# Optimization experiments

Measured on AMD Instinct MI355X. Metric: run time of the kernel, lower is better.

The kernel has to match this reference:

```python
import jax, jax.numpy as jnp
import numpy as np

E = 768
H = 12
D = E // H
K = 512  # max_relative_positions
SCALE = 1.0 / np.sqrt(3.0 * D)


def setup_inputs() -> dict:
    key = jax.random.key(0)
    ks = jax.random.split(key, 14)
    B, S = 4, 1024
    def lin(kw):
        return jax.random.normal(kw, (E, E), dtype=jnp.float32) * 0.02
    inp = {
        "x": jax.random.normal(ks[0], (B, S, E), dtype=jnp.float32),
        "Wq": lin(ks[1]), "bq": jnp.zeros((E,), jnp.float32),
        "Wk": lin(ks[2]), "bk": jnp.zeros((E,), jnp.float32),
        "Wv": lin(ks[3]), "bv": jnp.zeros((E,), jnp.float32),
        "Wpq": lin(ks[4]), "bpq": jnp.zeros((E,), jnp.float32),
        "Wpk": lin(ks[5]), "bpk": jnp.zeros((E,), jnp.float32),
        "rel_emb": jax.random.normal(ks[6], (2 * K + 1, E), dtype=jnp.float32) * 0.02,
        "Wo": lin(ks[7]), "bo": jnp.zeros((E,), jnp.float32),
    }
    return inp


def reference(x, Wq, bq, Wk, bk, Wv, bv, Wpq, bpq, Wpk, bpk, rel_emb, Wo, bo):
    B, S, _ = x.shape

    def split_heads(y):  # [B,S,E] -> [B,H,S,D]
        return y.reshape(B, S, H, D).transpose(0, 2, 1, 3)

    q_c = split_heads(x @ Wq.T + bq)
    k_c = split_heads(x @ Wk.T + bk)
    v = split_heads(x @ Wv.T + bv)

    # positional projections: [2K+1, E] -> [H, 2K+1, D]
    q_r = (rel_emb @ Wpq.T + bpq).reshape(2 * K + 1, H, D).transpose(1, 0, 2)
    k_r = (rel_emb @ Wpk.T + bpk).reshape(2 * K + 1, H, D).transpose(1, 0, 2)

    # relative index: rel[i, j] = clip(j - i, -K, K) + K
    pos = jnp.arange(S)
    rel = jnp.clip(pos[None, :] - pos[:, None], -K, K) + K  # [S, S] int32
    rel_b = jnp.broadcast_to(rel[None, None], (B, H, S, S))

    # content-to-content: [B,H,S,S]
    attn_cc = jnp.einsum('bhid,bhjd->bhij', q_c, k_c)

    # content-to-position: scores over all 2K+1 rel positions, then gather
    cp_score = jnp.einsum('bhid,hjd->bhij', q_c, k_r)  # [B,H,S,2K+1]
    attn_cp = jnp.take_along_axis(cp_score, rel_b, axis=-1)  # [B,H,S,S]

    # position-to-content: gather along last dim then transpose (i<->j)
    pc_score = jnp.einsum('bhjd,hkd->bhjk', k_c, q_r)  # [B,H,S,2K+1]
    attn_pc = jnp.take_along_axis(pc_score, rel_b, axis=-1).swapaxes(-1, -2)

    scores = (attn_cc + attn_cp + attn_pc) * SCALE
    weights = jax.nn.softmax(scores, axis=-1)

    ctx = jnp.einsum('bhij,bhjd->bhid', weights, v)
    ctx = ctx.transpose(0, 2, 1, 3).reshape(B, S, E)
    return ctx @ Wo.T + bo
```

## Files before the change

### kernel.cpp

```cpp
#include <hip/hip_runtime.h>
#include <stdint.h>

typedef __attribute__((ext_vector_type(8))) short bf8_t;
typedef __attribute__((ext_vector_type(4))) float f4_t;

#define DEV __device__ __forceinline__

constexpr int S_ = 1024;
constexpr float SCALE2_ = 0.104117584f;

DEV float bf2f(unsigned short u) { union { unsigned int i; float f; } v; v.i = ((unsigned int)u) << 16; return v.f; }
DEV unsigned short f2bf(float f) {
  union { float fv; unsigned int i; } v; v.fv = f;
  unsigned int r = v.i + 0x7FFFu + ((v.i >> 16) & 1u);
  return (unsigned short)(r >> 16);
}

DEV void gll16(const unsigned short* g, unsigned short* l) {
  __builtin_amdgcn_global_load_lds(
      (const __attribute__((address_space(1))) unsigned int*)g,
      (__attribute__((address_space(3))) unsigned int*)l, 16, 0, 0);
}

DEV const bf8_t* chunk128(const unsigned short* base, int row, int ck) {
  return (const bf8_t*)((const char*)base + row * 128 + (((ck ^ row) & 7) << 4));
}

struct CvtArgs { const float* src[8]; unsigned short* dst[8]; int nchunks[8]; };

__global__ __launch_bounds__(256) void cvt_kernel(CvtArgs a, int total) {
  int idx = blockIdx.x * 256 + threadIdx.x;
  int step = gridDim.x * 256;
  for (; idx < total; idx += step) {
    int c = idx, s = 0;
    while (c >= a.nchunks[s]) { c -= a.nchunks[s]; ++s; }
    float4 v = ((const float4*)a.src[s])[c];
    ushort4 o;
    o.x = f2bf(v.x); o.y = f2bf(v.y); o.z = f2bf(v.z); o.w = f2bf(v.w);
    ((ushort4*)a.dst[s])[c] = o;
  }
}

__global__ __launch_bounds__(256) void gemm_qkvrel(
    const unsigned short* __restrict__ xb, const unsigned short* __restrict__ Wqkv,
    const unsigned short* __restrict__ relb, const unsigned short* __restrict__ Wrel,
    unsigned short* __restrict__ Cqkv, unsigned short* __restrict__ Crel,
    const float* __restrict__ bq, const float* __restrict__ bk, const float* __restrict__ bv,
    const float* __restrict__ bpq, const float* __restrict__ bpk)
{
  __shared__ unsigned short At[64 * 64];
  __shared__ unsigned short Bt[128 * 64];
  const int tid = threadIdx.x, lane = tid & 63, w = tid >> 6;
  const int li = lane & 15, g = lane >> 4;
  const int wr = w >> 1, wc = w & 1;

  const int bid = blockIdx.x;
  const bool qkv = bid < 1152;
  const unsigned short *A, *B;
  int m0, n0, M, N;
  if (qkv) { m0 = (bid / 18) * 64; n0 = (bid % 18) * 128; A = xb;   B = Wqkv; M = 4096; N = 2304; }
  else     { int t = bid - 1152;
             m0 = (t / 12) * 64;  n0 = (t % 12) * 128;  A = relb; B = Wrel; M = 1025; N = 1536; }

  const int srow = tid >> 3;
  const int sl = (tid & 7) ^ (srow & 7);
  const long aoff0 = (long)min(m0 + srow,      M - 1) * 768 + sl * 8;
  const long aoff1 = (long)min(m0 + srow + 32, M - 1) * 768 + sl * 8;
  const long boff0 = (long)min(n0 + srow,      N - 1) * 768 + sl * 8;
  const long boff1 = (long)min(n0 + srow + 32, N - 1) * 768 + sl * 8;
  const long boff2 = (long)min(n0 + srow + 64, N - 1) * 768 + sl * 8;
  const long boff3 = (long)min(n0 + srow + 96, N - 1) * 768 + sl * 8;

  f4_t acc[2][4];
#pragma unroll
  for (int i = 0; i < 2; ++i)
#pragma unroll
    for (int j = 0; j < 4; ++j) acc[i][j] = f4_t{0.f, 0.f, 0.f, 0.f};

  for (int k0 = 0; k0 < 768; k0 += 64) {
    gll16(A + aoff0 + k0, At + tid * 8);
    gll16(A + aoff1 + k0, At + tid * 8 + 2048);
    gll16(B + boff0 + k0, Bt + tid * 8);
    gll16(B + boff1 + k0, Bt + tid * 8 + 2048);
    gll16(B + boff2 + k0, Bt + tid * 8 + 4096);
    gll16(B + boff3 + k0, Bt + tid * 8 + 6144);
    asm volatile("s_waitcnt vmcnt(0)" ::: "memory");
    __syncthreads();
#pragma unroll
    for (int ks = 0; ks < 2; ++ks) {
      bf8_t a[2], b[4];
#pragma unroll
      for (int fm = 0; fm < 2; ++fm)
        a[fm] = *chunk128(At, wr * 32 + fm * 16 + li, ks * 4 + g);
#pragma unroll
      for (int fn = 0; fn < 4; ++fn)
        b[fn] = *chunk128(Bt, wc * 64 + fn * 16 + li, ks * 4 + g);
#pragma unroll
      for (int fm = 0; fm < 2; ++fm)
#pragma unroll
        for (int fn = 0; fn < 4; ++fn)
          acc[fm][fn] = __builtin_amdgcn_mfma_f32_16x16x32_bf16(a[fm], b[fn], acc[fm][fn], 0, 0, 0);
    }
    __syncthreads();
  }

#pragma unroll
  for (int fm = 0; fm < 2; ++fm)
#pragma unroll
    for (int fn = 0; fn < 4; ++fn)
#pragma unroll
      for (int r = 0; r < 4; ++r) {
        int m = m0 + wr * 32 + fm * 16 + g * 4 + r;
        int n = n0 + wc * 64 + fn * 16 + li;
        if (m >= M || n >= N) continue;
        float v = acc[fm][fn][r];
        if (qkv) {
          int sel = (n >= 1536) ? 2 : (n >= 768 ? 1 : 0);
          int nn = n - sel * 768;
          v += (sel == 0 ? bq : sel == 1 ? bk : bv)[nn];
          long off = (long)sel * 3145728 + (long)((m >> 10) * 12 + (nn >> 6)) * 65536;
          if (sel == 2) off += (nn & 63) * 1024 + (m & 1023);
          else          off += (m & 1023) * 64 + (nn & 63);
          Cqkv[off] = f2bf(v);
        } else {
          int sel = n >= 768 ? 1 : 0;
          int nn = n - sel * 768;
          v += (sel ? bpk : bpq)[nn];
          long off = (long)sel * 787200 + (long)(nn >> 6) * 65600 + (long)m * 64 + (nn & 63);
          Crel[off] = f2bf(v);
        }
      }
}

__global__ __launch_bounds__(256) void gemm_out(
    const unsigned short* __restrict__ A,
    const unsigned short* __restrict__ B,
    float* __restrict__ C, const float* __restrict__ b0)
{
  __shared__ unsigned short At[64 * 64];
  __shared__ unsigned short Bt[128 * 64];
  const int tid = threadIdx.x, lane = tid & 63, w = tid >> 6;
  const int li = lane & 15, g = lane >> 4;
  const int wr = w >> 1, wc = w & 1;
  const int m0 = blockIdx.y * 64, n0 = blockIdx.x * 128;

  const int srow = tid >> 3;
  const int sl = (tid & 7) ^ (srow & 7);
  const long aoff0 = (long)(m0 + srow) * 768 + sl * 8;
  const long aoff1 = (long)(m0 + srow + 32) * 768 + sl * 8;
  const long boff0 = (long)(n0 + srow) * 768 + sl * 8;
  const long boff1 = (long)(n0 + srow + 32) * 768 + sl * 8;
  const long boff2 = (long)(n0 + srow + 64) * 768 + sl * 8;
  const long boff3 = (long)(n0 + srow + 96) * 768 + sl * 8;

  f4_t acc[2][4];
#pragma unroll
  for (int i = 0; i < 2; ++i)
#pragma unroll
    for (int j = 0; j < 4; ++j) acc[i][j] = f4_t{0.f, 0.f, 0.f, 0.f};

  for (int k0 = 0; k0 < 768; k0 += 64) {
    gll16(A + aoff0 + k0, At + tid * 8);
    gll16(A + aoff1 + k0, At + tid * 8 + 2048);
    gll16(B + boff0 + k0, Bt + tid * 8);
    gll16(B + boff1 + k0, Bt + tid * 8 + 2048);
    gll16(B + boff2 + k0, Bt + tid * 8 + 4096);
    gll16(B + boff3 + k0, Bt + tid * 8 + 6144);
    asm volatile("s_waitcnt vmcnt(0)" ::: "memory");
    __syncthreads();
#pragma unroll
    for (int ks = 0; ks < 2; ++ks) {
      bf8_t a[2], b[4];
#pragma unroll
      for (int fm = 0; fm < 2; ++fm)
        a[fm] = *chunk128(At, wr * 32 + fm * 16 + li, ks * 4 + g);
#pragma unroll
      for (int fn = 0; fn < 4; ++fn)
        b[fn] = *chunk128(Bt, wc * 64 + fn * 16 + li, ks * 4 + g);
#pragma unroll
      for (int fm = 0; fm < 2; ++fm)
#pragma unroll
        for (int fn = 0; fn < 4; ++fn)
          acc[fm][fn] = __builtin_amdgcn_mfma_f32_16x16x32_bf16(a[fm], b[fn], acc[fm][fn], 0, 0, 0);
    }
    __syncthreads();
  }

#pragma unroll
  for (int fm = 0; fm < 2; ++fm)
#pragma unroll
    for (int fn = 0; fn < 4; ++fn)
#pragma unroll
      for (int r = 0; r < 4; ++r) {
        int m = m0 + wr * 32 + fm * 16 + g * 4 + r;
        int n = n0 + wc * 64 + fn * 16 + li;
        C[(long)m * 768 + n] = acc[fm][fn][r] + b0[n];
      }
}

__global__ __launch_bounds__(256) void flash_kernel(
    const unsigned short* __restrict__ Q, const unsigned short* __restrict__ Kc,
    const unsigned short* __restrict__ kr, const unsigned short* __restrict__ qr,
    const unsigned short* __restrict__ Vt, unsigned short* __restrict__ ctx)
{
  const int flat = blockIdx.x;
  const int logical = (flat & 7) * 96 + (flat >> 3);
  const int bh = logical >> 4, h = bh % 12, bb = bh / 12;
  const int i0 = (logical & 15) * 64;
  const int tid = threadIdx.x, lane = tid & 63, w = tid >> 6;
  const int g = lane >> 4, li = lane & 15;
  const unsigned short* Qb  = Q  + (long)bh * (S_ * 64);
  const unsigned short* Kb  = Kc + (long)bh * (S_ * 64);
  const unsigned short* Vb  = Vt + (long)bh * (S_ * 64);
  const unsigned short* krh = kr + (long)h * 65600;
  const unsigned short* qrh = qr + (long)h * 65600;

  __shared__ unsigned short Kt[4096];
  __shared__ unsigned short Vl[4096];
  __shared__ unsigned short Tpc[64][132];
  __shared__ unsigned short TcpW[4][16][84];
  __shared__ unsigned short Pl[4096];

  const int mh = w & 1, nq = w >> 1;

  const int sr0 = w * 8 + (lane >> 3);
  const int scc = (lane & 7) ^ (sr0 & 7);
  auto stageK = [&](int jt) {
    const int j0n = jt * 64;
    gll16(Kb + (long)(j0n + sr0) * 64 + scc * 8,        &Kt[w * 512 + lane * 8]);
    gll16(Kb + (long)(j0n + sr0 + 32) * 64 + scc * 8,   &Kt[w * 512 + 2048 + lane * 8]);
  };
  auto stageV = [&](int jt) {
    const int j0n = jt * 64;
    gll16(Vb + (long)sr0 * 1024 + j0n + scc * 8,        &Vl[w * 512 + lane * 8]);
    gll16(Vb + (long)(sr0 + 32) * 1024 + j0n + scc * 8, &Vl[w * 512 + 2048 + lane * 8]);
  };

  bf8_t q3[2];
#pragma unroll
  for (int ks = 0; ks < 2; ++ks)
    q3[ks] = *(const bf8_t*)(Qb + (long)(i0 + w * 16 + li) * 64 + ks * 32 + g * 8);

  float l_p[4] = {0.f, 0.f, 0.f, 0.f};
  f4_t acc_o[4];
#pragma unroll
  for (int fn = 0; fn < 4; ++fn) acc_o[fn] = f4_t{0.f, 0.f, 0.f, 0.f};

  const int base_cp = li + 15 - g * 4;
  const int base_pc = 63 + w * 16 + g * 4 - li;

  stageK(0);
  stageV(0);

  for (int jt = 0; jt < 16; ++jt) {
    const int j0 = jt * 64;
    const int Dl = j0 - i0;
    const int wbU = Dl - w * 16 - 15 + 512;
    const int rbU = 449 - Dl;

    {
      f4_t at[5];
#pragma unroll
      for (int f5 = 0; f5 < 5; ++f5) at[f5] = f4_t{0.f, 0.f, 0.f, 0.f};
#pragma unroll
      for (int ks = 0; ks < 2; ++ks) {
        bf8_t b[5];
#pragma unroll
        for (int f5 = 0; f5 < 5; ++f5) {
          int krow = min(max(wbU + f5 * 16 + li, 0), 1024);
          b[f5] = *(const bf8_t*)(krh + (long)krow * 64 + ks * 32 + g * 8);
        }
        __builtin_amdgcn_s_setprio(1);
#pragma unroll
        for (int f5 = 0; f5 < 5; ++f5)
          at[f5] = __builtin_amdgcn_mfma_f32_16x16x32_bf16(q3[ks], b[f5], at[f5], 0, 0, 0);
        __builtin_amdgcn_s_setprio(0);
      }
#pragma unroll
      for (int f5 = 0; f5 < 5; ++f5)
#pragma unroll
        for (int r = 0; r < 4; ++r)
          TcpW[w][g * 4 + r][f5 * 16 + li] = f2bf(at[f5][r]);
    }

    asm volatile("s_waitcnt vmcnt(0)" ::: "memory");
    __builtin_amdgcn_s_barrier();

    f4_t s4[4];
#pragma unroll
    for (int fn = 0; fn < 4; ++fn) s4[fn] = f4_t{0.f, 0.f, 0.f, 0.f};

    {
      f4_t acc[2][4];
#pragma unroll
      for (int i = 0; i < 2; ++i)
#pragma unroll
        for (int j = 0; j < 4; ++j) acc[i][j] = f4_t{0.f, 0.f, 0.f, 0.f};
#pragma unroll
      for (int ks = 0; ks < 2; ++ks) {
        bf8_t a[2], b[4];
#pragma unroll
        for (int fm = 0; fm < 2; ++fm)
          a[fm] = *chunk128(Kt, mh * 32 + fm * 16 + li, ks * 4 + g);
#pragma unroll
        for (int fn = 0; fn < 4; ++fn) {
          int qrow = min(max(rbU + nq * 64 + fn * 16 + li, 0), 1024);
          b[fn] = *(const bf8_t*)(qrh + (long)qrow * 64 + ks * 32 + g * 8);
        }
        __builtin_amdgcn_s_setprio(1);
#pragma unroll
        for (int fm = 0; fm < 2; ++fm)
#pragma unroll
          for (int fn = 0; fn < 4; ++fn)
            acc[fm][fn] = __builtin_amdgcn_mfma_f32_16x16x32_bf16(a[fm], b[fn], acc[fm][fn], 0, 0, 0);
        __builtin_amdgcn_s_setprio(0);
      }
#pragma unroll
      for (int fm = 0; fm < 2; ++fm)
#pragma unroll
        for (int fn = 0; fn < 4; ++fn)
#pragma unroll
          for (int r = 0; r < 4; ++r)
            Tpc[mh * 32 + fm * 16 + g * 4 + r][nq * 64 + fn * 16 + li] = f2bf(acc[fm][fn][r]);

#pragma unroll
      for (int ks = 0; ks < 2; ++ks) {
        bf8_t b[4];
#pragma unroll
        for (int fn = 0; fn < 4; ++fn)
          b[fn] = *chunk128(Kt, fn * 16 + li, ks * 4 + g);
        __builtin_amdgcn_s_setprio(1);
#pragma unroll
        for (int fn = 0; fn < 4; ++fn)
          s4[fn] = __builtin_amdgcn_mfma_f32_16x16x32_bf16(q3[ks], b[fn], s4[fn], 0, 0, 0);
        __builtin_amdgcn_s_setprio(0);
      }
    }

    asm volatile("s_waitcnt lgkmcnt(0)" ::: "memory");
    __builtin_amdgcn_s_barrier();

    if (jt + 1 < 16) stageK(jt + 1);

#pragma unroll
    for (int fn = 0; fn < 4; ++fn)
#pragma unroll
      for (int r = 0; r < 4; ++r) {
        float v = s4[fn][r] + bf2f(TcpW[w][g * 4 + r][base_cp + fn * 16 - r])
                            + bf2f(Tpc[fn * 16 + li][base_pc + r - fn * 16]);
        float p = exp2f(v * SCALE2_);
        l_p[r] += p;
        const int row = w * 16 + g * 4 + r;
        int byte = row * 128 + (fn * 16 + li) * 2;
        byte ^= (row & 7) << 4;
        *(unsigned short*)((char*)Pl + byte) = f2bf(p);
      }

#pragma unroll
    for (int ks = 0; ks < 2; ++ks) {
      const int arow = w * 16 + li;
      int abyte = arow * 128 + ks * 64 + g * 16;
      abyte ^= (arow & 7) << 4;
      bf8_t a = *(const bf8_t*)((const char*)Pl + abyte);
      bf8_t b[4];
#pragma unroll
      for (int fn2 = 0; fn2 < 4; ++fn2)
        b[fn2] = *chunk128(Vl, fn2 * 16 + li, ks * 4 + g);
      __builtin_amdgcn_s_setprio(1);
#pragma unroll
      for (int fn2 = 0; fn2 < 4; ++fn2)
        acc_o[fn2] = __builtin_amdgcn_mfma_f32_16x16x32_bf16(a, b[fn2], acc_o[fn2], 0, 0, 0);
      __builtin_amdgcn_s_setprio(0);
    }

    if (jt + 1 < 16) {
      __builtin_amdgcn_s_barrier();
      stageV(jt + 1);
    }
  }

#pragma unroll
  for (int r = 0; r < 4; ++r)
#pragma unroll
    for (int off = 1; off < 16; off <<= 1) l_p[r] += __shfl_xor(l_p[r], off);
  float inv[4];
#pragma unroll
  for (int r = 0; r < 4; ++r) inv[r] = 1.0f / l_p[r];
#pragma unroll
  for (int fn2 = 0; fn2 < 4; ++fn2)
#pragma unroll
    for (int r = 0; r < 4; ++r) {
      const int row = i0 + w * 16 + g * 4 + r;
      const int d = fn2 * 16 + li;
      float v = acc_o[fn2][r] * inv[r];
      ctx[((long)bb * 1024 + row) * 768 + h * 64 + d] = f2bf(v);
    }
}

extern "C" void kernel_launch(void* const* d_in, const int* in_sizes, int n_in,
                              void* d_out, int out_size, void* d_ws, size_t ws_size,
                              hipStream_t stream)
{
  const float* x   = (const float*)d_in[0];
  const float* Wq  = (const float*)d_in[1];
  const float* bq  = (const float*)d_in[2];
  const float* Wk  = (const float*)d_in[3];
  const float* bk  = (const float*)d_in[4];
  const float* Wv  = (const float*)d_in[5];
  const float* bv  = (const float*)d_in[6];
  const float* Wpq = (const float*)d_in[7];
  const float* bpq = (const float*)d_in[8];
  const float* Wpk = (const float*)d_in[9];
  const float* bpk = (const float*)d_in[10];
  const float* rel = (const float*)d_in[11];
  const float* Wo  = (const float*)d_in[12];
  const float* bo  = (const float*)d_in[13];

  char* ws = (char*)d_ws;
  auto alloc = [&](size_t bytes) { char* p = ws; ws += (bytes + 255) & ~(size_t)255; return p; };
  unsigned short* xb   = (unsigned short*)alloc((size_t)4096 * 768 * 2);
  unsigned short* Wqb  = (unsigned short*)alloc((size_t)768 * 768 * 2);
  unsigned short* Wkb  = (unsigned short*)alloc((size_t)768 * 768 * 2);
  unsigned short* Wvb  = (unsigned short*)alloc((size_t)768 * 768 * 2);
  unsigned short* Wpqb = (unsigned short*)alloc((size_t)768 * 768 * 2);
  unsigned short* Wpkb = (unsigned short*)alloc((size_t)768 * 768 * 2);
  unsigned short* Wob  = (unsigned short*)alloc((size_t)768 * 768 * 2);
  unsigned short* relb = (unsigned short*)alloc((size_t)1025 * 768 * 2);
  unsigned short* Qb   = (unsigned short*)alloc((size_t)48 * 1024 * 64 * 2);
  unsigned short* Kb   = (unsigned short*)alloc((size_t)48 * 1024 * 64 * 2);
  unsigned short* Vt   = (unsigned short*)alloc((size_t)48 * 64 * 1024 * 2);
  unsigned short* qkx  = (unsigned short*)alloc((size_t)2 * 12 * 1025 * 64 * 2);
  unsigned short* ctx  = (unsigned short*)alloc((size_t)4096 * 768 * 2);

  CvtArgs ca;
  const float* srcs[8] = {x, Wq, Wk, Wv, Wpq, Wpk, Wo, rel};
  unsigned short* dsts[8] = {xb, Wqb, Wkb, Wvb, Wpqb, Wpkb, Wob, relb};
  const int nch[8] = {786432, 147456, 147456, 147456, 147456, 147456, 147456, 196800};
  int total = 0;
  for (int i = 0; i < 8; ++i) { ca.src[i] = srcs[i]; ca.dst[i] = dsts[i]; ca.nchunks[i] = nch[i]; total += nch[i]; }
  cvt_kernel<<<dim3(2048), dim3(256), 0, stream>>>(ca, total);

  dim3 blk(256);
  gemm_qkvrel<<<dim3(1356), blk, 0, stream>>>(xb, Wqb, relb, Wpqb, Qb, qkx,
                                              bq, bk, bv, bpq, bpk);
  flash_kernel<<<dim3(768), blk, 0, stream>>>(Qb, Kb, qkx + 787200, qkx, Vt, ctx);
  gemm_out<<<dim3(6, 64), blk, 0, stream>>>(ctx, Wob, (float*)d_out, bo);

  (void)in_sizes; (void)n_in; (void)out_size; (void)ws_size;
}
```

Measured before the change: 189.1 us.

## Double-buffer V tiles and reuse per-wave TcpW scratch for P staging

```diff
diff --git a/kernel.cpp b/kernel.cpp
--- a/kernel.cpp
+++ b/kernel.cpp
@@ -216,12 +216,12 @@
   const unsigned short* qrh = qr + (long)h * 65600;
 
   __shared__ unsigned short Kt[4096];
-  __shared__ unsigned short Vl[4096];
+  __shared__ unsigned short Vl[2][4096];
   __shared__ unsigned short Tpc[64][132];
   __shared__ unsigned short TcpW[4][16][84];
-  __shared__ unsigned short Pl[4096];
 
   const int mh = w & 1, nq = w >> 1;
+  unsigned short* PlW = &TcpW[w][0][0];
 
   const int sr0 = w * 8 + (lane >> 3);
   const int scc = (lane & 7) ^ (sr0 & 7);
@@ -230,10 +230,10 @@
     gll16(Kb + (long)(j0n + sr0) * 64 + scc * 8,        &Kt[w * 512 + lane * 8]);
     gll16(Kb + (long)(j0n + sr0 + 32) * 64 + scc * 8,   &Kt[w * 512 + 2048 + lane * 8]);
   };
-  auto stageV = [&](int jt) {
+  auto stageV = [&](int buf, int jt) {
     const int j0n = jt * 64;
-    gll16(Vb + (long)sr0 * 1024 + j0n + scc * 8,        &Vl[w * 512 + lane * 8]);
-    gll16(Vb + (long)(sr0 + 32) * 1024 + j0n + scc * 8, &Vl[w * 512 + 2048 + lane * 8]);
+    gll16(Vb + (long)sr0 * 1024 + j0n + scc * 8,        &Vl[buf][w * 512 + lane * 8]);
+    gll16(Vb + (long)(sr0 + 32) * 1024 + j0n + scc * 8, &Vl[buf][w * 512 + 2048 + lane * 8]);
   };
 
   bf8_t q3[2];
@@ -250,9 +250,10 @@
   const int base_pc = 63 + w * 16 + g * 4 - li;
 
   stageK(0);
-  stageV(0);
+  stageV(0, 0);
 
   for (int jt = 0; jt < 16; ++jt) {
+    const int cur = jt & 1;
     const int j0 = jt * 64;
     const int Dl = j0 - i0;
     const int wbU = Dl - w * 16 - 15 + 512;
@@ -340,8 +341,9 @@
     asm volatile("s_waitcnt lgkmcnt(0)" ::: "memory");
     __builtin_amdgcn_s_barrier();
 
-    if (jt + 1 < 16) stageK(jt + 1);
-
+    if (jt + 1 < 16) { stageK(jt + 1); stageV(cur ^ 1, jt + 1); }
+
+    float sc[4][4];
 #pragma unroll
     for (int fn = 0; fn < 4; ++fn)
 #pragma unroll
@@ -350,32 +352,32 @@
                             + bf2f(Tpc[fn * 16 + li][base_pc + r - fn * 16]);
         float p = exp2f(v * SCALE2_);
         l_p[r] += p;
-        const int row = w * 16 + g * 4 + r;
-        int byte = row * 128 + (fn * 16 + li) * 2;
-        byte ^= (row & 7) << 4;
-        *(unsigned short*)((char*)Pl + byte) = f2bf(p);
+        sc[fn][r] = p;
+      }
+
+#pragma unroll
+    for (int fn = 0; fn < 4; ++fn)
+#pragma unroll
+      for (int r = 0; r < 4; ++r) {
+        int byte = (g * 4 + r) * 128 + (fn * 16 + li) * 2;
+        byte ^= ((g * 4 + r) & 7) << 4;
+        *(unsigned short*)((char*)PlW + byte) = f2bf(sc[fn][r]);
       }
 
 #pragma unroll
     for (int ks = 0; ks < 2; ++ks) {
-      const int arow = w * 16 + li;
-      int abyte = arow * 128 + ks * 64 + g * 16;
-      abyte ^= (arow & 7) << 4;
-      bf8_t a = *(const bf8_t*)((const char*)Pl + abyte);
+      int abyte = li * 128 + ks * 64 + g * 16;
+      abyte ^= (li & 7) << 4;
+      bf8_t a = *(const bf8_t*)((const char*)PlW + abyte);
       bf8_t b[4];
 #pragma unroll
       for (int fn2 = 0; fn2 < 4; ++fn2)
-        b[fn2] = *chunk128(Vl, fn2 * 16 + li, ks * 4 + g);
+        b[fn2] = *chunk128(Vl[cur], fn2 * 16 + li, ks * 4 + g);
       __builtin_amdgcn_s_setprio(1);
 #pragma unroll
       for (int fn2 = 0; fn2 < 4; ++fn2)
         acc_o[fn2] = __builtin_amdgcn_mfma_f32_16x16x32_bf16(a, b[fn2], acc_o[fn2], 0, 0, 0);
       __builtin_amdgcn_s_setprio(0);
-    }
-
-    if (jt + 1 < 16) {
-      __builtin_amdgcn_s_barrier();
-      stageV(jt + 1);
     }
   }
 
```

Measured after the change: 189.8 us. Within noise of the previous version (+0.4%).
